# Kernel optimization log

Measured on AMD Instinct MI355X. Metric: run time of the kernel, lower is better.

## Reference

```python
import jax, jax.numpy as jnp
import numpy as np

DN = jax.lax.conv_dimension_numbers((1, 32, 32, 32, 1), (3, 3, 3, 1, 32), ('NDHWC', 'DHWIO', 'NDHWC'))


def setup_inputs() -> dict:
    key = jax.random.key(0)
    k0, k1, k2, k3, k4 = jax.random.split(key, 5)
    B = 64
    x = jax.random.normal(k0, (B, 32, 32, 32, 1), dtype=jnp.float32)
    # conv weights in DHWIO layout; kaiming-ish scale
    w1 = jax.random.normal(k1, (3, 3, 3, 1, 32), dtype=jnp.float32) * (1.0 / np.sqrt(27 * 1))
    b1 = jax.random.normal(k2, (32,), dtype=jnp.float32) * 0.01
    w2 = jax.random.normal(k3, (3, 3, 3, 32, 64), dtype=jnp.float32) * (1.0 / np.sqrt(27 * 32))
    b2 = jax.random.normal(k4, (64,), dtype=jnp.float32) * 0.01
    return {"x": x, "w1": w1, "b1": b1, "w2": w2, "b2": b2}


def _conv3d_valid(x, w):
    # x: [B, D, H, W, C_in], w: [kD, kH, kW, C_in, C_out] -> [B, D-2, H-2, W-2, C_out]
    dn = jax.lax.conv_dimension_numbers(x.shape, w.shape, ('NDHWC', 'DHWIO', 'NDHWC'))
    return jax.lax.conv_general_dilated(x, w, window_strides=(1, 1, 1),
                                        padding='VALID', dimension_numbers=dn)


def reference(x, w1, b1, w2, b2):
    # Dense input -> all voxels active, so spconv's gather-GEMM-scatter equals
    # a dense valid 3D conv. ReLU acts on active-site features == dense ReLU.
    h = jax.nn.relu(_conv3d_valid(x, w1) + b1)        # [B, 30, 30, 30, 32]
    h = jax.nn.relu(_conv3d_valid(h, w2) + b2)        # [B, 28, 28, 28, 64]
    # spconv ToDense returns NCDHW
    return jnp.transpose(h, (0, 4, 1, 2, 3))          # [B, 64, 28, 28, 28]
```

## Files before the change

kernel.cpp:

```cpp
#include <hip/hip_runtime.h>
#include <cstdint>
#include <cstddef>

typedef __attribute__((ext_vector_type(8))) short bf16x8;
typedef __attribute__((ext_vector_type(4))) float f32x4;
typedef __attribute__((ext_vector_type(4))) unsigned int u32x4;
typedef unsigned short u16;

#define H1_ROW_B   1920
#define H1_BATCH   (30 * 30 * 960)
#define LDS_STRIDE 1952
#define OUT_CSTR   21952

__device__ __forceinline__ u16 f2bf(float f) {
    union { float f; unsigned u; } v; v.f = f;
    unsigned r = v.u + 0x7FFF + ((v.u >> 16) & 1);
    return (u16)(r >> 16);
}

__device__ __forceinline__ void fma4(float4& a, float s, const float4& w) {
    a.x = fmaf(s, w.x, a.x);
    a.y = fmaf(s, w.y, a.y);
    a.z = fmaf(s, w.z, a.z);
    a.w = fmaf(s, w.w, a.w);
}

__global__ __launch_bounds__(256) void conv1_relu(
    const float* __restrict__ x, const float* __restrict__ w1,
    const float* __restrict__ b1, u16* __restrict__ h1, int b0)
{
    __shared__ float wl[27 * 32 + 32];

    const int z   = blockIdx.x;
    const int yt  = blockIdx.y;
    const int bl  = blockIdx.z;
    const int b   = b0 + bl;
    const int tid = threadIdx.x;

    for (int i = tid; i < 27 * 32; i += 256) wl[i] = w1[i];
    if (tid < 32) wl[27 * 32 + tid] = b1[tid];
    __syncthreads();

    const int c4    = tid & 7;
    const int xslot = tid >> 3;

    const float4 bias = *reinterpret_cast<const float4*>(&wl[27 * 32 + c4 * 4]);
    const float* xb  = x + (size_t)b * 32768;
    u16*         h1b = h1 + (size_t)bl * H1_BATCH;

#pragma unroll 1
    for (int j = 0; j < 6; ++j) {
        const int s = xslot + 32 * j;
        if (s >= 180) break;
        const int yy = s / 30;
        const int xx = s - yy * 30;
        const int y  = yt * 6 + yy;

        float4 acc = bias;
#pragma unroll
        for (int kd = 0; kd < 3; ++kd) {
#pragma unroll
            for (int kh = 0; kh < 3; ++kh) {
                const float* row = xb + ((size_t)(z + kd) * 32 + (y + kh)) * 32 + xx;
                const float a0 = row[0], a1 = row[1], a2 = row[2];
                const int t = (kd * 3 + kh) * 3;
                const float4 w0  = *reinterpret_cast<const float4*>(&wl[(t + 0) * 32 + c4 * 4]);
                const float4 w1v = *reinterpret_cast<const float4*>(&wl[(t + 1) * 32 + c4 * 4]);
                const float4 w2v = *reinterpret_cast<const float4*>(&wl[(t + 2) * 32 + c4 * 4]);
                fma4(acc, a0, w0);
                fma4(acc, a1, w1v);
                fma4(acc, a2, w2v);
            }
        }
        ushort4 st;
        st.x = f2bf(fmaxf(acc.x, 0.f));
        st.y = f2bf(fmaxf(acc.y, 0.f));
        st.z = f2bf(fmaxf(acc.z, 0.f));
        st.w = f2bf(fmaxf(acc.w, 0.f));
        *reinterpret_cast<ushort4*>(
            h1b + ((size_t)(z * 30 + y) * 30 + xx) * 32 + c4 * 4) = st;
    }
}

__global__ __launch_bounds__(256) void pack_w2(
    const float* __restrict__ w2, u16* __restrict__ wB)
{
    const int tap = blockIdx.x;
    const int tid = threadIdx.x;
    const int nt = tid >> 6;
    const int l  = tid & 63;
    const int r = l & 15, q = l >> 4;
    u16* dst = wB + ((size_t)(tap * 4 + nt) * 64 + l) * 8;
#pragma unroll
    for (int j = 0; j < 8; ++j)
        dst[j] = f2bf(w2[(size_t)(tap * 32 + q * 8 + j) * 64 + nt * 16 + r]);
}

__global__ __launch_bounds__(512, 4) void conv2_mfma(
    const u16* __restrict__ h1, const u16* __restrict__ wB,
    const float* __restrict__ b2, float* __restrict__ out, int b0)
{
    __shared__ __align__(16) unsigned char smem[36 * LDS_STRIDE];

    const int g   = gridDim.x;
    const int bid = blockIdx.x;
    const int lb  = (g % 8 == 0) ? ((bid & 7) * (g >> 3) + (bid >> 3)) : bid;

    const int t0  = lb % 49;
    const int bl  = lb / 49;
    const int yg  = t0 % 7;
    const int zt  = t0 / 7;

    const int b  = b0 + bl;
    const int y0 = yg * 4, z0 = zt * 4;
    const int tid = threadIdx.x;
    const int wv  = tid >> 6;
    const int l   = tid & 63;
    const int zw  = wv >> 1;
    const int nh  = wv & 1;
    const int r = l & 15, q = l >> 4;
    const int yl = r >> 2, xg = r & 3;

    const char* wBl = (const char*)wB + nh * 2048 + l * 16;

    {
        const char* gbase = (const char*)(h1 + (size_t)bl * H1_BATCH);
        for (int c = wv; c < 72; c += 8) {
            const int rid = c >> 1, half = c & 1;
            const int zz = rid / 6, yy = rid - zz * 6;
            const char* src = gbase
                + (size_t)((z0 + zz) * 30 + (y0 + yy)) * H1_ROW_B
                + half * 896 + l * 16;
            unsigned char* dst = smem + rid * LDS_STRIDE + half * 896 + l * 16;
            __builtin_amdgcn_global_load_lds(
                (const __attribute__((address_space(1))) void*)src,
                (__attribute__((address_space(3))) void*)dst, 16, 0, 0);
        }
    }
    __syncthreads();

    f32x4 acc[7][2];
    {
        const float bv0 = b2[nh * 32 + r];
        const float bv1 = b2[nh * 32 + 16 + r];
#pragma unroll
        for (int mt = 0; mt < 7; ++mt) {
            acc[mt][0] = (f32x4){bv0, bv0, bv0, bv0};
            acc[mt][1] = (f32x4){bv1, bv1, bv1, bv1};
        }
    }

    const unsigned char* aBase =
        smem + (zw * 6 + yl) * LDS_STRIDE + xg * 64 + q * 16;

    u32x4 Bs[2][2];
#define B_LOAD(slot, t)                                                        \
    { const char* p_ = wBl + (size_t)(t) * 4096;                               \
      asm volatile("global_load_dwordx4 %0, %2, off\n\t"                       \
                   "global_load_dwordx4 %1, %2, off offset:1024"               \
                   : "=&v"(Bs[slot][0]), "=&v"(Bs[slot][1]) : "v"(p_)); }

    B_LOAD(0, 0)

#pragma unroll
    for (int tap = 0; tap < 27; ++tap) {
        const int cur = tap & 1;

        if (tap < 26) B_LOAD(cur ^ 1, tap + 1)

        if (tap < 26) asm volatile("s_waitcnt vmcnt(2)");
        else          asm volatile("s_waitcnt vmcnt(0)");

        asm volatile("" : "+v"(Bs[cur][0]), "+v"(Bs[cur][1]));
        const bf16x8 B0 = __builtin_bit_cast(bf16x8, Bs[cur][0]);
        const bf16x8 B1 = __builtin_bit_cast(bf16x8, Bs[cur][1]);

        const int kd = tap / 9;
        const int kh = (tap - kd * 9) / 3;
        const int kw = tap - kd * 9 - kh * 3;
        const unsigned char* ap = aBase + (kd * 6 + kh) * LDS_STRIDE + kw * 64;

        __builtin_amdgcn_s_setprio(1);
#pragma unroll
        for (int mt = 0; mt < 7; ++mt) {
            const bf16x8 a = *reinterpret_cast<const bf16x8*>(ap + mt * 256);
            acc[mt][0] = __builtin_amdgcn_mfma_f32_16x16x32_bf16(a, B0, acc[mt][0], 0, 0, 0);
            acc[mt][1] = __builtin_amdgcn_mfma_f32_16x16x32_bf16(a, B1, acc[mt][1], 0, 0, 0);
        }
        __builtin_amdgcn_s_setprio(0);
    }
#undef B_LOAD

    const int z = z0 + zw;
    float* ob = out + ((size_t)b * 64 + nh * 32 + r) * OUT_CSTR
                    + (size_t)z * 784 + (size_t)(y0 + q) * 28;
#pragma unroll
    for (int mt = 0; mt < 7; ++mt) {
#pragma unroll
        for (int nt = 0; nt < 2; ++nt) {
            const f32x4 v = acc[mt][nt];
            float4 st;
            st.x = fmaxf(v.x, 0.f);
            st.y = fmaxf(v.y, 0.f);
            st.z = fmaxf(v.z, 0.f);
            st.w = fmaxf(v.w, 0.f);
            *reinterpret_cast<float4*>(ob + (size_t)nt * 16 * OUT_CSTR + mt * 4) = st;
        }
    }
}

extern "C" void kernel_launch(void* const* d_in, const int* in_sizes, int n_in,
                              void* d_out, int out_size, void* d_ws, size_t ws_size,
                              hipStream_t stream)
{
    const float* x  = (const float*)d_in[0];
    const float* w1 = (const float*)d_in[1];
    const float* b1 = (const float*)d_in[2];
    const float* w2 = (const float*)d_in[3];
    const float* b2 = (const float*)d_in[4];
    float* out = (float*)d_out;

    u16* wB = (u16*)d_ws;
    u16* h1 = (u16*)((char*)d_ws + 131072);

    pack_w2<<<27, 256, 0, stream>>>(w2, wB);

    const size_t per_batch = (size_t)H1_BATCH * 2;
    size_t avail = ws_size > 131072 ? ws_size - 131072 : 0;
    int bchunk = (int)(avail / per_batch);
    if (bchunk < 1)  bchunk = 1;
    if (bchunk > 64) bchunk = 64;

    for (int b0 = 0; b0 < 64; b0 += bchunk) {
        int bc = 64 - b0;
        if (bc > bchunk) bc = bchunk;
        conv1_relu<<<dim3(30, 5, bc), 256, 0, stream>>>(x, w1, b1, h1, b0);
        conv2_mfma<<<dim3(49 * bc), 512, 0, stream>>>(h1, wB, b2, out, b0);
    }
}
```

Baseline: 270.2 us.

## Widen conv2 waves to all 64 channels and register-block conv1 over x pairs

conv2 now runs 4 waves per block, each covering all 64 output channels (4 N-tiles). Previously 8 waves split channels in halves. This lets each LDS A-fragment feed four MFMAs instead of two, halving A reads per MFMA, at the cost of more accumulator and B registers and fewer waves per block. conv1 now has each thread compute two adjacent x outputs, sharing input loads and weight LDS reads, and leaves 16 threads per block idle.

```diff
diff --git a/kernel.cpp b/kernel.cpp
--- a/kernel.cpp
+++ b/kernel.cpp
@@ -41,44 +41,50 @@
     if (tid < 32) wl[27 * 32 + tid] = b1[tid];
     __syncthreads();
 
-    const int c4    = tid & 7;
-    const int xslot = tid >> 3;
+    const int c4   = tid & 7;
+    const int slot = tid >> 3;
 
     const float4 bias = *reinterpret_cast<const float4*>(&wl[27 * 32 + c4 * 4]);
     const float* xb  = x + (size_t)b * 32768;
     u16*         h1b = h1 + (size_t)bl * H1_BATCH;
 
+    if (slot < 30) {
 #pragma unroll 1
-    for (int j = 0; j < 6; ++j) {
-        const int s = xslot + 32 * j;
-        if (s >= 180) break;
-        const int yy = s / 30;
-        const int xx = s - yy * 30;
-        const int y  = yt * 6 + yy;
-
-        float4 acc = bias;
-#pragma unroll
-        for (int kd = 0; kd < 3; ++kd) {
-#pragma unroll
-            for (int kh = 0; kh < 3; ++kh) {
-                const float* row = xb + ((size_t)(z + kd) * 32 + (y + kh)) * 32 + xx;
-                const float a0 = row[0], a1 = row[1], a2 = row[2];
-                const int t = (kd * 3 + kh) * 3;
-                const float4 w0  = *reinterpret_cast<const float4*>(&wl[(t + 0) * 32 + c4 * 4]);
-                const float4 w1v = *reinterpret_cast<const float4*>(&wl[(t + 1) * 32 + c4 * 4]);
-                const float4 w2v = *reinterpret_cast<const float4*>(&wl[(t + 2) * 32 + c4 * 4]);
-                fma4(acc, a0, w0);
-                fma4(acc, a1, w1v);
-                fma4(acc, a2, w2v);
+        for (int j = 0; j < 3; ++j) {
+            const int p  = slot + 30 * j;
+            const int yy = p / 15;
+            const int xx = (p - yy * 15) * 2;
+            const int y  = yt * 6 + yy;
+
+            float4 acc0 = bias, acc1 = bias;
+#pragma unroll
+            for (int kd = 0; kd < 3; ++kd) {
+#pragma unroll
+                for (int kh = 0; kh < 3; ++kh) {
+                    const float* row = xb + ((size_t)(z + kd) * 32 + (y + kh)) * 32 + xx;
+                    const float2 v01 = *reinterpret_cast<const float2*>(row);
+                    const float2 v23 = *reinterpret_cast<const float2*>(row + 2);
+                    const int t = (kd * 3 + kh) * 3;
+                    const float4 w0  = *reinterpret_cast<const float4*>(&wl[(t + 0) * 32 + c4 * 4]);
+                    const float4 w1v = *reinterpret_cast<const float4*>(&wl[(t + 1) * 32 + c4 * 4]);
+                    const float4 w2v = *reinterpret_cast<const float4*>(&wl[(t + 2) * 32 + c4 * 4]);
+                    fma4(acc0, v01.x, w0);
+                    fma4(acc0, v01.y, w1v);
+                    fma4(acc0, v23.x, w2v);
+                    fma4(acc1, v01.y, w0);
+                    fma4(acc1, v23.x, w1v);
+                    fma4(acc1, v23.y, w2v);
+                }
             }
-        }
-        ushort4 st;
-        st.x = f2bf(fmaxf(acc.x, 0.f));
-        st.y = f2bf(fmaxf(acc.y, 0.f));
-        st.z = f2bf(fmaxf(acc.z, 0.f));
-        st.w = f2bf(fmaxf(acc.w, 0.f));
-        *reinterpret_cast<ushort4*>(
-            h1b + ((size_t)(z * 30 + y) * 30 + xx) * 32 + c4 * 4) = st;
+            ushort4 s0, s1;
+            s0.x = f2bf(fmaxf(acc0.x, 0.f)); s0.y = f2bf(fmaxf(acc0.y, 0.f));
+            s0.z = f2bf(fmaxf(acc0.z, 0.f)); s0.w = f2bf(fmaxf(acc0.w, 0.f));
+            s1.x = f2bf(fmaxf(acc1.x, 0.f)); s1.y = f2bf(fmaxf(acc1.y, 0.f));
+            s1.z = f2bf(fmaxf(acc1.z, 0.f)); s1.w = f2bf(fmaxf(acc1.w, 0.f));
+            u16* dst = h1b + ((size_t)(z * 30 + y) * 30 + xx) * 32 + c4 * 4;
+            *reinterpret_cast<ushort4*>(dst)      = s0;
+            *reinterpret_cast<ushort4*>(dst + 32) = s1;
+        }
     }
 }
 
@@ -96,7 +102,7 @@
         dst[j] = f2bf(w2[(size_t)(tap * 32 + q * 8 + j) * 64 + nt * 16 + r]);
 }
 
-__global__ __launch_bounds__(512, 4) void conv2_mfma(
+__global__ __launch_bounds__(256, 2) void conv2_mfma(
     const u16* __restrict__ h1, const u16* __restrict__ wB,
     const float* __restrict__ b2, float* __restrict__ out, int b0)
 {
@@ -116,16 +122,14 @@
     const int tid = threadIdx.x;
     const int wv  = tid >> 6;
     const int l   = tid & 63;
-    const int zw  = wv >> 1;
-    const int nh  = wv & 1;
     const int r = l & 15, q = l >> 4;
     const int yl = r >> 2, xg = r & 3;
 
-    const char* wBl = (const char*)wB + nh * 2048 + l * 16;
+    const char* wBl = (const char*)wB + l * 16;
 
     {
         const char* gbase = (const char*)(h1 + (size_t)bl * H1_BATCH);
-        for (int c = wv; c < 72; c += 8) {
+        for (int c = wv; c < 72; c += 4) {
             const int rid = c >> 1, half = c & 1;
             const int zz = rid / 6, yy = rid - zz * 6;
             const char* src = gbase
@@ -139,26 +143,34 @@
     }
     __syncthreads();
 
-    f32x4 acc[7][2];
+    f32x4 acc[7][4];
     {
-        const float bv0 = b2[nh * 32 + r];
-        const float bv1 = b2[nh * 32 + 16 + r];
+        const float bv0 = b2[r];
+        const float bv1 = b2[16 + r];
+        const float bv2 = b2[32 + r];
+        const float bv3 = b2[48 + r];
 #pragma unroll
         for (int mt = 0; mt < 7; ++mt) {
             acc[mt][0] = (f32x4){bv0, bv0, bv0, bv0};
             acc[mt][1] = (f32x4){bv1, bv1, bv1, bv1};
+            acc[mt][2] = (f32x4){bv2, bv2, bv2, bv2};
+            acc[mt][3] = (f32x4){bv3, bv3, bv3, bv3};
         }
     }
 
     const unsigned char* aBase =
-        smem + (zw * 6 + yl) * LDS_STRIDE + xg * 64 + q * 16;
-
-    u32x4 Bs[2][2];
+        smem + (wv * 6 + yl) * LDS_STRIDE + xg * 64 + q * 16;
+
+    u32x4 Bs[2][4];
 #define B_LOAD(slot, t)                                                        \
     { const char* p_ = wBl + (size_t)(t) * 4096;                               \
-      asm volatile("global_load_dwordx4 %0, %2, off\n\t"                       \
-                   "global_load_dwordx4 %1, %2, off offset:1024"               \
-                   : "=&v"(Bs[slot][0]), "=&v"(Bs[slot][1]) : "v"(p_)); }
+      asm volatile("global_load_dwordx4 %0, %4, off\n\t"                       \
+                   "global_load_dwordx4 %1, %4, off offset:1024\n\t"           \
+                   "global_load_dwordx4 %2, %4, off offset:2048\n\t"           \
+                   "global_load_dwordx4 %3, %4, off offset:3072"               \
+                   : "=&v"(Bs[slot][0]), "=&v"(Bs[slot][1]),                   \
+                     "=&v"(Bs[slot][2]), "=&v"(Bs[slot][3])                    \
+                   : "v"(p_)); }
 
     B_LOAD(0, 0)
 
@@ -168,12 +180,15 @@
 
         if (tap < 26) B_LOAD(cur ^ 1, tap + 1)
 
-        if (tap < 26) asm volatile("s_waitcnt vmcnt(2)");
+        if (tap < 26) asm volatile("s_waitcnt vmcnt(4)");
         else          asm volatile("s_waitcnt vmcnt(0)");
 
-        asm volatile("" : "+v"(Bs[cur][0]), "+v"(Bs[cur][1]));
+        asm volatile("" : "+v"(Bs[cur][0]), "+v"(Bs[cur][1]),
+                          "+v"(Bs[cur][2]), "+v"(Bs[cur][3]));
         const bf16x8 B0 = __builtin_bit_cast(bf16x8, Bs[cur][0]);
         const bf16x8 B1 = __builtin_bit_cast(bf16x8, Bs[cur][1]);
+        const bf16x8 B2 = __builtin_bit_cast(bf16x8, Bs[cur][2]);
+        const bf16x8 B3 = __builtin_bit_cast(bf16x8, Bs[cur][3]);
 
         const int kd = tap / 9;
         const int kh = (tap - kd * 9) / 3;
@@ -186,18 +201,20 @@
             const bf16x8 a = *reinterpret_cast<const bf16x8*>(ap + mt * 256);
             acc[mt][0] = __builtin_amdgcn_mfma_f32_16x16x32_bf16(a, B0, acc[mt][0], 0, 0, 0);
             acc[mt][1] = __builtin_amdgcn_mfma_f32_16x16x32_bf16(a, B1, acc[mt][1], 0, 0, 0);
+            acc[mt][2] = __builtin_amdgcn_mfma_f32_16x16x32_bf16(a, B2, acc[mt][2], 0, 0, 0);
+            acc[mt][3] = __builtin_amdgcn_mfma_f32_16x16x32_bf16(a, B3, acc[mt][3], 0, 0, 0);
         }
         __builtin_amdgcn_s_setprio(0);
     }
 #undef B_LOAD
 
-    const int z = z0 + zw;
-    float* ob = out + ((size_t)b * 64 + nh * 32 + r) * OUT_CSTR
+    const int z = z0 + wv;
+    float* ob = out + ((size_t)b * 64 + r) * OUT_CSTR
                     + (size_t)z * 784 + (size_t)(y0 + q) * 28;
 #pragma unroll
     for (int mt = 0; mt < 7; ++mt) {
 #pragma unroll
-        for (int nt = 0; nt < 2; ++nt) {
+        for (int nt = 0; nt < 4; ++nt) {
             const f32x4 v = acc[mt][nt];
             float4 st;
             st.x = fmaxf(v.x, 0.f);
@@ -235,6 +252,6 @@
         int bc = 64 - b0;
         if (bc > bchunk) bc = bchunk;
         conv1_relu<<<dim3(30, 5, bc), 256, 0, stream>>>(x, w1, b1, h1, b0);
-        conv2_mfma<<<dim3(49 * bc), 512, 0, stream>>>(h1, wB, b2, out, b0);
-    }
-}
+        conv2_mfma<<<dim3(49 * bc), 256, 0, stream>>>(h1, wB, b2, out, b0);
+    }
+}
```

New measurement: 295.5 us. 9.4% more time.
